# Kernel tuning notes

Measured on AMD Instinct MI355X. Metric: run time of the kernel, lower is better.

## Reference

```python
import jax, jax.numpy as jnp
import numpy as np

BEAM = 4
SOS = 1


def _gru_cell(x, h, Wih, Whh, bih, bhh):
    # x,h: [B,H]; Wih,Whh: [3H,H]; torch GRUCell math
    gi = x @ Wih.T + bih
    gh = h @ Whh.T + bhh
    ir, iz, inn = jnp.split(gi, 3, axis=-1)
    hr, hz, hn = jnp.split(gh, 3, axis=-1)
    r = jax.nn.sigmoid(ir + hr)
    z = jax.nn.sigmoid(iz + hz)
    n = jnp.tanh(inn + r * hn)
    return (1.0 - z) * n + z * h


def setup_inputs() -> dict:
    key = jax.random.key(0)
    V, H, S, L = 32000, 1024, 256, 48
    ks = jax.random.split(key, 10)
    p = lambda k, shape: (jax.random.normal(k, shape, jnp.float32) * 0.02)
    return {
        "input_seq": jax.random.randint(ks[0], (S, 1), 0, V),
        "input_length": S,
        "max_length": L,
        "emb": p(ks[1], (V, H)),
        "enc_Wih": p(ks[2], (3 * H, H)),
        "enc_Whh": p(ks[3], (3 * H, H)),
        "enc_bih": jnp.zeros((3 * H,), jnp.float32),
        "enc_bhh": jnp.zeros((3 * H,), jnp.float32),
        "dec_Wih": p(ks[4], (3 * H, H)),
        "dec_Whh": p(ks[5], (3 * H, H)),
        "dec_bih": jnp.zeros((3 * H,), jnp.float32),
        "dec_bhh": jnp.zeros((3 * H,), jnp.float32),
        "Wc": p(ks[6], (H, 2 * H)),
        "Wout": p(ks[7], (V, H)),
    }


def _beam_search(input_seq, max_length, emb, enc_Wih, enc_Whh, enc_bih, enc_bhh,
                 dec_Wih, dec_Whh, dec_bih, dec_bhh, Wc, Wout):
    H = emb.shape[1]
    # ---- encoder: single-layer GRU over [S] tokens ----
    seq_emb = emb[input_seq[:, 0]]  # [S,H]

    def enc_step(h, x):
        hn = _gru_cell(x[None, :], h, enc_Wih, enc_Whh, enc_bih, enc_bhh)
        return hn, hn[0]

    h0 = jnp.zeros((1, H), emb.dtype)
    h_final, enc_out = jax.lax.scan(enc_step, h0, seq_emb)  # enc_out: [S,H]

    # ---- beam state (all beams start from encoder final hidden, SOS token) ----
    h = jnp.tile(h_final, (BEAM, 1))            # [4,H]
    inputs = jnp.full((BEAM,), SOS, jnp.int32)  # [4]
    cum = jnp.zeros((BEAM,), emb.dtype)
    tokens = jnp.zeros((BEAM, max_length), jnp.int32)
    shist = jnp.zeros((BEAM, max_length), emb.dtype)

    def dec_step(carry, step):
        h, inputs, cum, tokens, shist = carry
        x = emb[inputs]                                     # [4,H]
        hnew = _gru_cell(x, h, dec_Wih, dec_Whh, dec_bih, dec_bhh)  # [4,H]
        # Luong dot attention over encoder outputs
        attn = jax.nn.softmax(jnp.einsum('sh,bh->bs', enc_out, hnew), axis=-1)
        ctx = attn @ enc_out                                # [4,H]
        concat = jnp.tanh(jnp.concatenate([hnew, ctx], axis=-1) @ Wc.T)
        logp = jax.nn.log_softmax(concat @ Wout.T, axis=-1)  # [4,V]
        tp, ti = jax.lax.top_k(logp, BEAM)                  # [4,4]
        # step 0: only beam 0 expands (all beams identical), as in original
        valid = jnp.where(step == 0, jnp.arange(BEAM) == 0,
                          jnp.ones((BEAM,), bool))
        cand = jnp.where(valid[:, None], cum[:, None] + tp, -jnp.inf).reshape(-1)
        sel_scores, sel = jax.lax.top_k(cand, BEAM)         # [4]
        bi = sel // BEAM   # parent beam index i
        jj = sel % BEAM    # topk column index j
        # Faithful to original bug: new hidden indexed by column j, not parent i
        new_h = hnew[jj]
        new_inputs = ti[bi, jj]
        step_scores = tp[bi, jj]
        new_tokens = tokens[bi].at[:, step].set(new_inputs)
        new_shist = shist[bi].at[:, step].set(step_scores)
        return (new_h, new_inputs, sel_scores, new_tokens, new_shist), None

    (h, inputs, cum, tokens, shist), _ = jax.lax.scan(
        dec_step, (h, inputs, cum, tokens, shist), jnp.arange(max_length))
    best = jnp.argmax(cum)  # all beams same length -> avg == cum ranking
    return tokens[best], shist[best]


def reference(input_seq, input_length, max_length, emb, enc_Wih, enc_Whh,
              enc_bih, enc_bhh, dec_Wih, dec_Whh, dec_bih, dec_bhh, Wc, Wout):
    # input_length: full sequence is used (original packs to input_length;
    # here input_length == seq_len)
    return _beam_search(input_seq, max_length, emb, enc_Wih, enc_Whh, enc_bih,
                        enc_bhh, dec_Wih, dec_Whh, dec_bih, dec_bhh, Wc, Wout)
```

## Files before the change

kernel.cpp:

```cpp
#include <hip/hip_runtime.h>
#include <hip/hip_bf16.h>

#define HDIM 1024
#define G3   3072
#define CHK  16
#define NEG_INF (-__builtin_inff())

typedef unsigned short u16;
typedef unsigned int   u32;

__device__ __forceinline__ float bf2f(u32 h){ union{u32 u; float f;} t; t.u = h<<16; return t.f; }

__device__ __forceinline__ float wred_sum(float v){
  #pragma unroll
  for(int o=32;o;o>>=1) v += __shfl_xor(v,o,64);
  return v;
}
__device__ __forceinline__ float wred_max(float v){
  #pragma unroll
  for(int o=32;o;o>>=1) v = fmaxf(v,__shfl_xor(v,o,64));
  return v;
}

__device__ __forceinline__ void load16w(const void* W, long long eoff, int bf, float* x){
  if(bf){
    const uint4* q = (const uint4*)((const u16*)W + eoff);
    uint4 a = q[0], b = q[1];
    x[0]=bf2f(a.x&0xffffu); x[1]=bf2f(a.x>>16);
    x[2]=bf2f(a.y&0xffffu); x[3]=bf2f(a.y>>16);
    x[4]=bf2f(a.z&0xffffu); x[5]=bf2f(a.z>>16);
    x[6]=bf2f(a.w&0xffffu); x[7]=bf2f(a.w>>16);
    x[8]=bf2f(b.x&0xffffu); x[9]=bf2f(b.x>>16);
    x[10]=bf2f(b.y&0xffffu); x[11]=bf2f(b.y>>16);
    x[12]=bf2f(b.z&0xffffu); x[13]=bf2f(b.z>>16);
    x[14]=bf2f(b.w&0xffffu); x[15]=bf2f(b.w>>16);
  } else {
    const float4* q = (const float4*)((const float*)W + eoff);
    float4 A=q[0],B=q[1],C=q[2],D=q[3];
    x[0]=A.x;x[1]=A.y;x[2]=A.z;x[3]=A.w;
    x[4]=B.x;x[5]=B.y;x[6]=B.z;x[7]=B.w;
    x[8]=C.x;x[9]=C.y;x[10]=C.z;x[11]=C.w;
    x[12]=D.x;x[13]=D.y;x[14]=D.z;x[15]=D.w;
  }
}
__device__ __forceinline__ void load16f(const float* p, float* x){
  const float4* q=(const float4*)p;
  float4 A=q[0],B=q[1],C=q[2],D=q[3];
  x[0]=A.x;x[1]=A.y;x[2]=A.z;x[3]=A.w;
  x[4]=B.x;x[5]=B.y;x[6]=B.z;x[7]=B.w;
  x[8]=C.x;x[9]=C.y;x[10]=C.z;x[11]=C.w;
  x[12]=D.x;x[13]=D.y;x[14]=D.z;x[15]=D.w;
}
__device__ __forceinline__ float loadscal(const void* p, long long i, int bf){
  return bf ? bf2f(((const u16*)p)[i]) : ((const float*)p)[i];
}
__device__ __forceinline__ float sigf(float x){ return 1.f/(1.f+expf(-x)); }

__device__ __forceinline__ void dot4_accum(const float* w, const float xr[4][16], float a[4]){
  #pragma unroll
  for(int i=0;i<16;i++){
    a[0] += w[i]*xr[0][i];
    a[1] += w[i]*xr[1][i];
    a[2] += w[i]*xr[2][i];
    a[3] += w[i]*xr[3][i];
  }
}

__device__ __forceinline__ void insert4(float* v, int* ix, float nv, int ni){
  bool b3 = (nv>v[3]) || (nv==v[3] && ni<ix[3]);
  if(!b3) return;
  bool b2 = (nv>v[2]) || (nv==v[2] && ni<ix[2]);
  bool b1 = (nv>v[1]) || (nv==v[1] && ni<ix[1]);
  bool b0 = (nv>v[0]) || (nv==v[0] && ni<ix[0]);
  if(b0){ v[3]=v[2];ix[3]=ix[2]; v[2]=v[1];ix[2]=ix[1]; v[1]=v[0];ix[1]=ix[0]; v[0]=nv;ix[0]=ni; }
  else if(b1){ v[3]=v[2];ix[3]=ix[2]; v[2]=v[1];ix[2]=ix[1]; v[1]=nv;ix[1]=ni; }
  else if(b2){ v[3]=v[2];ix[3]=ix[2]; v[2]=nv;ix[2]=ni; }
  else { v[3]=nv; ix[3]=ni; }
}
__device__ __forceinline__ void merge4(const float* va, const int* ia, const float* vb, const int* ib, float* vo, int* io){
  int pa=0, pb=0;
  for(int k=0;k<4;k++){
    bool ta;
    if(pa>=4) ta=false;
    else if(pb>=4) ta=true;
    else ta = (va[pa]>vb[pb]) || (va[pa]==vb[pb] && ia[pa]<ib[pb]);
    if(ta){ vo[k]=va[pa]; io[k]=ia[pa]; pa++; }
    else  { vo[k]=vb[pb]; io[k]=ib[pb]; pb++; }
  }
}

__global__ __launch_bounds__(256) void k_probe(const u16* emb, int* flag){
  __shared__ int cnt;
  if(threadIdx.x==0) cnt=0;
  __syncthreads();
  int c=0;
  for(int i=threadIdx.x;i<4096;i+=256){
    u32 e = (emb[i]>>7)&0xffu;
    if(e>=0x85u) c++;
  }
  atomicAdd(&cnt,c);
  __syncthreads();
  if(threadIdx.x==0) *flag = (cnt<100)?1:0;
}

__global__ __launch_bounds__(256) void k_enc_gi(const int* seq, const void* emb, const void* Wih,
                                                const void* bih, const int* flag, float* gi){
  int bf = *flag;
  int wg = blockIdx.x; int tg = wg>>3, rg = wg&7;
  int wave = threadIdx.x>>6, lane = threadIdx.x&63;
  int tok[4];
  #pragma unroll
  for(int j=0;j<4;j++) tok[j] = seq[tg*4+j];
  float xr[4][16];
  #pragma unroll
  for(int j=0;j<4;j++) load16w(emb, (long long)tok[j]*HDIM + lane*CHK, bf, xr[j]);
  for(int k=0;k<96;k++){
    int row = rg*384 + wave*96 + k;
    float w[16]; load16w(Wih, (long long)row*HDIM + lane*CHK, bf, w);
    float a[4]={0.f,0.f,0.f,0.f};
    dot4_accum(w, xr, a);
    float bias = loadscal(bih, row, bf);
    #pragma unroll
    for(int b=0;b<4;b++){
      float v = wred_sum(a[b]);
      if(lane==b) gi[(long long)(tg*4+b)*G3 + row] = v + bias;
    }
  }
}

__global__ __launch_bounds__(256) void k_enc_step(const void* Whh, const void* bhh, const int* flag,
                                                  const float* gi, float* enc_out, int t){
  int bf = *flag;
  __shared__ float gh[96];
  int wave = threadIdx.x>>6, lane = threadIdx.x&63;
  int base = blockIdx.x*32;
  float xr[16];
  if(t>0){
    load16f(enc_out + (long long)(t-1)*HDIM + lane*CHK, xr);
  } else {
    #pragma unroll
    for(int i=0;i<16;i++) xr[i]=0.f;
  }
  for(int k=0;k<24;k++){
    int idx = wave*24+k;
    int g = idx>>5, d = idx&31;
    int row = g*HDIM + base + d;
    float w[16]; load16w(Whh,(long long)row*HDIM+lane*CHK,bf,w);
    float a=0.f;
    #pragma unroll
    for(int i=0;i<16;i++) a += w[i]*xr[i];
    a = wred_sum(a);
    if(lane==0) gh[idx] = a + loadscal(bhh,row,bf);
  }
  __syncthreads();
  if(threadIdx.x<32){
    int d = threadIdx.x;
    const float* gir = gi + (long long)t*G3;
    float ir = gir[base+d], iz = gir[HDIM+base+d], in_ = gir[2*HDIM+base+d];
    float hr = gh[d], hz = gh[32+d], hn = gh[64+d];
    float r = sigf(ir+hr);
    float z = sigf(iz+hz);
    float n = tanhf(in_ + r*hn);
    float hp = (t>0) ? enc_out[(long long)(t-1)*HDIM + base+d] : 0.f;
    enc_out[(long long)t*HDIM + base+d] = (1.f-z)*n + z*hp;
  }
}

__global__ __launch_bounds__(256) void k_dec_init(const float* enc_out, int S, float* h_cur, float* cum,
                                                  int* cur_in, int* tokens, float* shist, int L){
  int t = threadIdx.x;
  const float* hf = enc_out + (long long)(S-1)*HDIM;
  for(int i=t;i<4*HDIM;i+=256) h_cur[i] = hf[i&(HDIM-1)];
  if(t<4){ cum[t]=0.f; cur_in[t]=1; }
  for(int i=t;i<4*L;i+=256){ tokens[i]=0; shist[i]=0.f; }
}

__global__ __launch_bounds__(256) void k_dec_gru(const void* emb, const void* Wih, const void* Whh,
                                                 const void* bih, const void* bhh, const int* flag,
                                                 const int* cur_in, const float* h_cur, float* hnew){
  int bf = *flag;
  __shared__ float gibuf[96], ghbuf[96];
  int wave = threadIdx.x>>6, lane = threadIdx.x&63;
  int base = blockIdx.x*8;
  float xr[4][16];
  int tok[4];
  #pragma unroll
  for(int b=0;b<4;b++) tok[b]=cur_in[b];
  #pragma unroll
  for(int b=0;b<4;b++) load16w(emb,(long long)tok[b]*HDIM+lane*CHK,bf,xr[b]);
  for(int k=0;k<6;k++){
    int idx = wave*6+k; int g = idx>>3, d = idx&7;
    int row = g*HDIM + base + d;
    float w[16]; load16w(Wih,(long long)row*HDIM+lane*CHK,bf,w);
    float a[4]={0.f,0.f,0.f,0.f};
    dot4_accum(w,xr,a);
    float bias = loadscal(bih,row,bf);
    #pragma unroll
    for(int b=0;b<4;b++){
      float v = wred_sum(a[b]);
      if(lane==b) gibuf[idx*4+b] = v + bias;
    }
  }
  #pragma unroll
  for(int b=0;b<4;b++) load16f(h_cur+(long long)b*HDIM+lane*CHK, xr[b]);
  for(int k=0;k<6;k++){
    int idx = wave*6+k; int g = idx>>3, d = idx&7;
    int row = g*HDIM + base + d;
    float w[16]; load16w(Whh,(long long)row*HDIM+lane*CHK,bf,w);
    float a[4]={0.f,0.f,0.f,0.f};
    dot4_accum(w,xr,a);
    float bias = loadscal(bhh,row,bf);
    #pragma unroll
    for(int b=0;b<4;b++){
      float v = wred_sum(a[b]);
      if(lane==b) ghbuf[idx*4+b] = v + bias;
    }
  }
  __syncthreads();
  if(threadIdx.x<32){
    int d = threadIdx.x&7, b = threadIdx.x>>3;
    float ir = gibuf[(0*8+d)*4+b], iz = gibuf[(1*8+d)*4+b], in_ = gibuf[(2*8+d)*4+b];
    float hr = ghbuf[(0*8+d)*4+b], hz = ghbuf[(1*8+d)*4+b], hn = ghbuf[(2*8+d)*4+b];
    float r = sigf(ir+hr);
    float z = sigf(iz+hz);
    float n = tanhf(in_ + r*hn);
    float h = h_cur[b*HDIM + base + d];
    hnew[b*HDIM + base + d] = (1.f-z)*n + z*h;
  }
}

__global__ __launch_bounds__(256) void k_dec_scores(const float* enc_out, const float* hnew, float* scores){
  int wave = threadIdx.x>>6, lane = threadIdx.x&63;
  float xr[4][16];
  #pragma unroll
  for(int b=0;b<4;b++) load16f(hnew+(long long)b*HDIM+lane*CHK, xr[b]);
  for(int k=0;k<4;k++){
    int s = (blockIdx.x*4+wave)*4+k;
    float w[16]; load16f(enc_out+(long long)s*HDIM+lane*CHK, w);
    float a[4]={0.f,0.f,0.f,0.f};
    dot4_accum(w,xr,a);
    #pragma unroll
    for(int b=0;b<4;b++){
      float v = wred_sum(a[b]);
      if(lane==b) scores[s*4+b] = v;
    }
  }
}

__global__ __launch_bounds__(256) void k_dec_attnctx(const float* enc_out, const float* scores_g,
                                                     float* ctx, int S){
  __shared__ float sc[256*4];
  int t = threadIdx.x;
  for(int i=t;i<S*4;i+=256) sc[i]=scores_g[i];
  __syncthreads();
  int wave = t>>6, lane = t&63;
  {
    int b = wave;
    float v[4];
    #pragma unroll
    for(int k=0;k<4;k++) v[k]=sc[(lane+64*k)*4+b];
    float m = fmaxf(fmaxf(v[0],v[1]),fmaxf(v[2],v[3]));
    m = wred_max(m);
    float e[4]; float ss=0.f;
    #pragma unroll
    for(int k=0;k<4;k++){ e[k]=expf(v[k]-m); ss+=e[k]; }
    ss = wred_sum(ss);
    #pragma unroll
    for(int k=0;k<4;k++) sc[(lane+64*k)*4+b] = e[k]/ss;
  }
  __syncthreads();
  int hl = t&127, bp = t>>7;
  int h = blockIdx.x*128 + hl;
  int b0 = bp*2;
  float a0=0.f, a1=0.f;
  for(int s=0;s<S;s++){
    float e = enc_out[(long long)s*HDIM + h];
    a0 += sc[s*4+b0]*e;
    a1 += sc[s*4+b0+1]*e;
  }
  ctx[b0*HDIM+h]=a0; ctx[(b0+1)*HDIM+h]=a1;
}

__global__ __launch_bounds__(256) void k_dec_wc(const void* Wc, const int* flag, const float* hnew,
                                                const float* ctx, float* concat){
  int bf = *flag;
  int wave = threadIdx.x>>6, lane = threadIdx.x&63;
  int r0 = blockIdx.x*16 + wave*4;
  float xr[4][16];
  #pragma unroll
  for(int b=0;b<4;b++) load16f(hnew+(long long)b*HDIM+lane*CHK, xr[b]);
  float acc[4][4];
  #pragma unroll
  for(int k=0;k<4;k++){
    #pragma unroll
    for(int b=0;b<4;b++) acc[k][b]=0.f;
  }
  #pragma unroll
  for(int k=0;k<4;k++){
    float w[16]; load16w(Wc,(long long)(r0+k)*2048 + lane*CHK, bf, w);
    #pragma unroll
    for(int i=0;i<16;i++){
      acc[k][0]+=w[i]*xr[0][i]; acc[k][1]+=w[i]*xr[1][i];
      acc[k][2]+=w[i]*xr[2][i]; acc[k][3]+=w[i]*xr[3][i];
    }
  }
  #pragma unroll
  for(int b=0;b<4;b++) load16f(ctx+(long long)b*HDIM+lane*CHK, xr[b]);
  #pragma unroll
  for(int k=0;k<4;k++){
    float w[16]; load16w(Wc,(long long)(r0+k)*2048 + 1024 + lane*CHK, bf, w);
    #pragma unroll
    for(int i=0;i<16;i++){
      acc[k][0]+=w[i]*xr[0][i]; acc[k][1]+=w[i]*xr[1][i];
      acc[k][2]+=w[i]*xr[2][i]; acc[k][3]+=w[i]*xr[3][i];
    }
  }
  #pragma unroll
  for(int k=0;k<4;k++){
    #pragma unroll
    for(int b=0;b<4;b++){
      float v = wred_sum(acc[k][b]);
      if(lane == k*4+b) concat[b*HDIM + r0 + k] = tanhf(v);
    }
  }
}

__global__ __launch_bounds__(256) void k_dec_logits(const void* Wout, const int* flag, const float* concat,
                                                    float* pm, float* ps, float* ptv, int* pti, int V){
  int bf = *flag;
  int wave = threadIdx.x>>6, lane = threadIdx.x&63;
  float xr[4][16];
  #pragma unroll
  for(int b=0;b<4;b++) load16f(concat+(long long)b*HDIM+lane*CHK, xr[b]);
  int wbase = blockIdx.x*125;
  int off = wave*31 + (wave>0?1:0);
  int cnt = (wave==0)?32:31;
  float m[4], s[4], tv[4][4]; int ti_[4][4];
  #pragma unroll
  for(int b=0;b<4;b++){
    m[b]=NEG_INF; s[b]=0.f;
    #pragma unroll
    for(int j=0;j<4;j++){ tv[b][j]=NEG_INF; ti_[b][j]=0; }
  }
  for(int k=0;k<cnt;k++){
    int row = wbase + off + k;
    if(row>=V) break;
    float w[16]; load16w(Wout,(long long)row*HDIM+lane*CHK,bf,w);
    float a[4]={0.f,0.f,0.f,0.f};
    dot4_accum(w,xr,a);
    a[0]=wred_sum(a[0]); a[1]=wred_sum(a[1]); a[2]=wred_sum(a[2]); a[3]=wred_sum(a[3]);
    if(lane==0){
      #pragma unroll
      for(int b=0;b<4;b++){
        float v = a[b];
        if(v>m[b]){ s[b]=s[b]*expf(m[b]-v)+1.f; m[b]=v; }
        else s[b] += expf(v-m[b]);
        insert4(tv[b], ti_[b], v, row);
      }
    }
  }
  __shared__ float lm[16], lssum[16], ltv[64]; __shared__ int lti[64];
  if(lane==0){
    #pragma unroll
    for(int b=0;b<4;b++){
      lm[wave*4+b]=m[b]; lssum[wave*4+b]=s[b];
      #pragma unroll
      for(int j=0;j<4;j++){ ltv[(wave*4+b)*4+j]=tv[b][j]; lti[(wave*4+b)*4+j]=ti_[b][j]; }
    }
  }
  __syncthreads();
  if(threadIdx.x==0){
    for(int b=0;b<4;b++){
      float M=NEG_INF;
      for(int w=0;w<4;w++) M=fmaxf(M,lm[w*4+b]);
      float S=0.f;
      for(int w=0;w<4;w++) S += lssum[w*4+b]*expf(lm[w*4+b]-M);
      float cv[4]; int ci[4];
      for(int j=0;j<4;j++){ cv[j]=ltv[(0*4+b)*4+j]; ci[j]=lti[(0*4+b)*4+j]; }
      for(int w=1;w<4;w++){
        float vo[4]; int io[4];
        merge4(cv,ci,&ltv[(w*4+b)*4],&lti[(w*4+b)*4],vo,io);
        for(int j=0;j<4;j++){ cv[j]=vo[j]; ci[j]=io[j]; }
      }
      pm[blockIdx.x*4+b]=M; ps[blockIdx.x*4+b]=S;
      for(int j=0;j<4;j++){ ptv[(blockIdx.x*4+b)*4+j]=cv[j]; pti[(blockIdx.x*4+b)*4+j]=ci[j]; }
    }
  }
}

__global__ __launch_bounds__(256) void k_dec_finalize(const float* pm, const float* ps, const float* ptv,
                                                      const int* pti, const float* hnew, float* h_cur,
                                                      float* cum, int* cur_in, int* tokens, float* shist,
                                                      int step, int L, const int* flag, void* dout){
  __shared__ float red[256];
  __shared__ float tpv[4][4]; __shared__ int tpi[4][4];
  __shared__ float logZ[4];
  __shared__ float mtv[256*4]; __shared__ int mti[256*4];
  __shared__ int l_bi[4], l_jj[4], l_tok[4]; __shared__ float l_ss[4], l_cum[4];
  __shared__ int otok[4*64]; __shared__ float oshi[4*64];
  __shared__ int bbest;
  int t = threadIdx.x;

  for(int b=0;b<4;b++){
    float v = pm[t*4+b];
    red[t]=v; __syncthreads();
    for(int st=128;st;st>>=1){ if(t<st) red[t]=fmaxf(red[t],red[t+st]); __syncthreads(); }
    float M = red[0]; __syncthreads();
    red[t] = ps[t*4+b]*expf(v-M); __syncthreads();
    for(int st=128;st;st>>=1){ if(t<st) red[t]+=red[t+st]; __syncthreads(); }
    if(t==0) logZ[b]=M+logf(red[0]);
    __syncthreads();
  }
  for(int b=0;b<4;b++){
    for(int j=0;j<4;j++){ mtv[t*4+j]=ptv[(t*4+b)*4+j]; mti[t*4+j]=pti[(t*4+b)*4+j]; }
    __syncthreads();
    for(int st=1; st<256; st<<=1){
      if((t & (2*st-1))==0 && t+st<256){
        float vo[4]; int io[4];
        merge4(&mtv[t*4], &mti[t*4], &mtv[(t+st)*4], &mti[(t+st)*4], vo, io);
        for(int j=0;j<4;j++){ mtv[t*4+j]=vo[j]; mti[t*4+j]=io[j]; }
      }
      __syncthreads();
    }
    if(t<4){ tpv[b][t]=mtv[t]-logZ[b]; tpi[b][t]=mti[t]; }
    __syncthreads();
  }
  if(t==0){
    float oc[4];
    for(int b=0;b<4;b++) oc[b]=cum[b];
    float cand[16];
    for(int b=0;b<4;b++)
      for(int j=0;j<4;j++){
        bool valid = (step>0)||(b==0);
        cand[b*4+j] = valid ? oc[b]+tpv[b][j] : NEG_INF;
      }
    bool used[16];
    for(int i=0;i<16;i++) used[i]=false;
    for(int q=0;q<4;q++){
      int best=0; float bv=NEG_INF;
      for(int i=0;i<16;i++){ if(!used[i] && cand[i]>bv){ bv=cand[i]; best=i; } }
      used[best]=true;
      int bi = best>>2, jj = best&3;
      l_bi[q]=bi; l_jj[q]=jj; l_tok[q]=tpi[bi][jj]; l_ss[q]=tpv[bi][jj]; l_cum[q]=bv;
    }
  }
  __syncthreads();
  for(int i=t;i<4*L;i+=256){ otok[i]=tokens[i]; oshi[i]=shist[i]; }
  __syncthreads();
  for(int i=t;i<4*L;i+=256){
    int q=i/L, c=i%L;
    int src=l_bi[q];
    tokens[i] = (c==step)? l_tok[q] : otok[src*L+c];
    shist[i]  = (c==step)? l_ss[q]  : oshi[src*L+c];
  }
  if(t<4){ cum[t]=l_cum[t]; cur_in[t]=l_tok[t]; }
  for(int i=t;i<4*HDIM;i+=256){
    int q=i>>10;
    h_cur[i] = hnew[l_jj[q]*HDIM + (i&(HDIM-1))];
  }
  if(step==L-1){
    if(t==0){
      int bb=0; float bv=l_cum[0];
      for(int b=1;b<4;b++) if(l_cum[b]>bv){ bv=l_cum[b]; bb=b; }
      bbest=bb;
    }
    __syncthreads();
    int bb=bbest; int bf=*flag;
    for(int c=t;c<L;c+=256){
      float tokv = (float)((c==step)? l_tok[bb] : otok[l_bi[bb]*L+c]);
      float shv  = (c==step)? l_ss[bb] : oshi[l_bi[bb]*L+c];
      if(bf){
        __hip_bfloat16* o = (__hip_bfloat16*)dout;
        o[c]   = __float2bfloat16(tokv);
        o[L+c] = __float2bfloat16(shv);
      } else {
        float* o = (float*)dout;
        o[c]   = tokv;
        o[L+c] = shv;
      }
    }
  }
}

extern "C" void kernel_launch(void* const* d_in, const int* in_sizes, int n_in,
                              void* d_out, int out_size, void* d_ws, size_t ws_size,
                              hipStream_t stream) {
  const int* seq   = (const int*)d_in[0];
  const void* emb  = d_in[3];
  const void* eWih = d_in[4]; const void* eWhh = d_in[5];
  const void* ebih = d_in[6]; const void* ebhh = d_in[7];
  const void* dWih = d_in[8]; const void* dWhh = d_in[9];
  const void* dbih = d_in[10]; const void* dbhh = d_in[11];
  const void* Wc   = d_in[12]; const void* Wout = d_in[13];

  int S = in_sizes[0];
  int L = out_size/2;
  int V = in_sizes[13]/HDIM;

  char* p = (char*)d_ws;
  auto carve = [&](size_t bytes)->void* {
    void* r = (void*)p;
    p += (bytes + 255) & ~(size_t)255;
    return r;
  };
  int*   flag    = (int*)  carve(4);
  float* gi_enc  = (float*)carve((size_t)S*G3*4);
  float* enc_out = (float*)carve((size_t)S*HDIM*4);
  float* h_cur   = (float*)carve(4*HDIM*4);
  float* hnew    = (float*)carve(4*HDIM*4);
  float* scoresb = (float*)carve((size_t)S*4*4);
  float* ctx     = (float*)carve(4*HDIM*4);
  float* concat  = (float*)carve(4*HDIM*4);
  float* pm      = (float*)carve(256*4*4);
  float* ps      = (float*)carve(256*4*4);
  float* ptv     = (float*)carve(256*16*4);
  int*   pti     = (int*)  carve(256*16*4);
  float* cum     = (float*)carve(4*4);
  int*   cur_in  = (int*)  carve(4*4);
  int*   tokens  = (int*)  carve(4*L*4);
  float* shist   = (float*)carve(4*L*4);

  k_probe<<<1,256,0,stream>>>((const u16*)emb, flag);
  k_enc_gi<<<(S/4)*8,256,0,stream>>>(seq, emb, eWih, ebih, flag, gi_enc);
  for(int t=0;t<S;t++)
    k_enc_step<<<32,256,0,stream>>>(eWhh, ebhh, flag, gi_enc, enc_out, t);
  k_dec_init<<<1,256,0,stream>>>(enc_out, S, h_cur, cum, cur_in, tokens, shist, L);
  for(int st=0;st<L;st++){
    k_dec_gru<<<128,256,0,stream>>>(emb, dWih, dWhh, dbih, dbhh, flag, cur_in, h_cur, hnew);
    k_dec_scores<<<16,256,0,stream>>>(enc_out, hnew, scoresb);
    k_dec_attnctx<<<8,256,0,stream>>>(enc_out, scoresb, ctx, S);
    k_dec_wc<<<64,256,0,stream>>>(Wc, flag, hnew, ctx, concat);
    k_dec_logits<<<256,256,0,stream>>>(Wout, flag, concat, pm, ps, ptv, pti, V);
    k_dec_finalize<<<1,256,0,stream>>>(pm, ps, ptv, pti, hnew, h_cur, cum, cur_in,
                                       tokens, shist, st, L, flag, d_out);
  }
}
```

Before: 11.59 ms.

## Replace per-step encoder launches with persistent grid-barrier kernel; widen logits blocks

The 256 per-timestep encoder GRU launches become one persistent kernel of 32 blocks of 512 threads. Each block keeps its 96 rows of Whh in registers and the blocks synchronise between timesteps with an atomic-counter grid barrier. This is meant to remove launch overhead and the repeated reload of Whh from memory at every step. It relies on all 32 blocks being resident at once, and the register-held weights raise register pressure. Separately, the logits kernel moves from 4 to 8 waves per block to spread its rows across more waves.

```diff
diff --git a/kernel.cpp b/kernel.cpp
--- a/kernel.cpp
+++ b/kernel.cpp
@@ -5,6 +5,7 @@
 #define G3   3072
 #define CHK  16
 #define NEG_INF (-__builtin_inff())
+#define EB   32
 
 typedef unsigned short u16;
 typedef unsigned int   u32;
@@ -89,9 +90,21 @@
   }
 }
 
-__global__ __launch_bounds__(256) void k_probe(const u16* emb, int* flag){
+__device__ __forceinline__ void gbar(int* cnt, int nblk, int it){
+  __syncthreads();
+  if(threadIdx.x==0){
+    __hip_atomic_fetch_add(cnt, 1, __ATOMIC_ACQ_REL, __HIP_MEMORY_SCOPE_AGENT);
+    int target = nblk*it;
+    while(__hip_atomic_load(cnt, __ATOMIC_ACQUIRE, __HIP_MEMORY_SCOPE_AGENT) < target)
+      __builtin_amdgcn_s_sleep(1);
+  }
+  __syncthreads();
+  __builtin_amdgcn_fence(__ATOMIC_ACQUIRE, "agent");
+}
+
+__global__ __launch_bounds__(256) void k_probe(const u16* emb, int* flag, int* bar_cnt){
   __shared__ int cnt;
-  if(threadIdx.x==0) cnt=0;
+  if(threadIdx.x==0){ cnt=0; *bar_cnt=0; }
   __syncthreads();
   int c=0;
   for(int i=threadIdx.x;i<4096;i+=256){
@@ -128,41 +141,58 @@
   }
 }
 
-__global__ __launch_bounds__(256) void k_enc_step(const void* Whh, const void* bhh, const int* flag,
-                                                  const float* gi, float* enc_out, int t){
+__global__ __launch_bounds__(512,2) void k_enc_persist(const void* Whh, const void* bhh,
+                                                       const int* flag, const float* gi,
+                                                       float* enc_out, int S, int* bar_cnt){
   int bf = *flag;
-  __shared__ float gh[96];
   int wave = threadIdx.x>>6, lane = threadIdx.x&63;
-  int base = blockIdx.x*32;
-  float xr[16];
-  if(t>0){
-    load16f(enc_out + (long long)(t-1)*HDIM + lane*CHK, xr);
-  } else {
-    #pragma unroll
-    for(int i=0;i<16;i++) xr[i]=0.f;
-  }
-  for(int k=0;k<24;k++){
-    int idx = wave*24+k;
-    int g = idx>>5, d = idx&31;
-    int row = g*HDIM + base + d;
-    float w[16]; load16w(Whh,(long long)row*HDIM+lane*CHK,bf,w);
-    float a=0.f;
-    #pragma unroll
-    for(int i=0;i<16;i++) a += w[i]*xr[i];
-    a = wred_sum(a);
-    if(lane==0) gh[idx] = a + loadscal(bhh,row,bf);
-  }
-  __syncthreads();
-  if(threadIdx.x<32){
-    int d = threadIdx.x;
-    const float* gir = gi + (long long)t*G3;
-    float ir = gir[base+d], iz = gir[HDIM+base+d], in_ = gir[2*HDIM+base+d];
-    float hr = gh[d], hz = gh[32+d], hn = gh[64+d];
-    float r = sigf(ir+hr);
-    float z = sigf(iz+hz);
-    float n = tanhf(in_ + r*hn);
-    float hp = (t>0) ? enc_out[(long long)(t-1)*HDIM + base+d] : 0.f;
-    enc_out[(long long)t*HDIM + base+d] = (1.f-z)*n + z*hp;
+  int dbase = blockIdx.x*32;
+  __shared__ float gh_s[96];
+  __shared__ float bhh_s[96];
+  if(threadIdx.x<96){
+    int rl = threadIdx.x;
+    int row = (rl>>5)*HDIM + dbase + (rl&31);
+    bhh_s[rl] = loadscal(bhh, row, bf);
+  }
+  float wreg[12][16];
+  #pragma unroll
+  for(int k=0;k<12;k++){
+    int rl = wave*12 + k;
+    int row = (rl>>5)*HDIM + dbase + (rl&31);
+    load16w(Whh, (long long)row*HDIM + lane*CHK, bf, wreg[k]);
+  }
+  __syncthreads();
+
+  for(int t=0;t<S;t++){
+    if(t>0) gbar(bar_cnt, EB, t);
+    float h[16];
+    if(t>0){
+      load16f(enc_out + (long long)(t-1)*HDIM + lane*CHK, h);
+    } else {
+      #pragma unroll
+      for(int i=0;i<16;i++) h[i]=0.f;
+    }
+    #pragma unroll
+    for(int k=0;k<12;k++){
+      float a=0.f;
+      #pragma unroll
+      for(int i=0;i<16;i++) a += wreg[k][i]*h[i];
+      a = wred_sum(a);
+      if(lane==k) gh_s[wave*12+k] = a + bhh_s[wave*12+k];
+    }
+    __syncthreads();
+    if(threadIdx.x<32){
+      int d = threadIdx.x;
+      int gd = dbase + d;
+      const float* gir = gi + (long long)t*G3;
+      float ir = gir[gd], iz = gir[HDIM+gd], in_ = gir[2*HDIM+gd];
+      float hr = gh_s[d], hz = gh_s[32+d], hn = gh_s[64+d];
+      float r = sigf(ir+hr);
+      float z = sigf(iz+hz);
+      float n = tanhf(in_ + r*hn);
+      float hp = (t>0) ? enc_out[(long long)(t-1)*HDIM + gd] : 0.f;
+      enc_out[(long long)t*HDIM + gd] = (1.f-z)*n + z*hp;
+    }
   }
 }
 
@@ -325,7 +355,7 @@
   }
 }
 
-__global__ __launch_bounds__(256) void k_dec_logits(const void* Wout, const int* flag, const float* concat,
+__global__ __launch_bounds__(512) void k_dec_logits(const void* Wout, const int* flag, const float* concat,
                                                     float* pm, float* ps, float* ptv, int* pti, int V){
   int bf = *flag;
   int wave = threadIdx.x>>6, lane = threadIdx.x&63;
@@ -333,8 +363,8 @@
   #pragma unroll
   for(int b=0;b<4;b++) load16f(concat+(long long)b*HDIM+lane*CHK, xr[b]);
   int wbase = blockIdx.x*125;
-  int off = wave*31 + (wave>0?1:0);
-  int cnt = (wave==0)?32:31;
+  int off  = (wave<5) ? wave*16 : 80 + (wave-5)*15;
+  int cnt  = (wave<5) ? 16 : 15;
   float m[4], s[4], tv[4][4]; int ti_[4][4];
   #pragma unroll
   for(int b=0;b<4;b++){
@@ -359,7 +389,7 @@
       }
     }
   }
-  __shared__ float lm[16], lssum[16], ltv[64]; __shared__ int lti[64];
+  __shared__ float lm[32], lssum[32], ltv[128]; __shared__ int lti[128];
   if(lane==0){
     #pragma unroll
     for(int b=0;b<4;b++){
@@ -372,12 +402,12 @@
   if(threadIdx.x==0){
     for(int b=0;b<4;b++){
       float M=NEG_INF;
-      for(int w=0;w<4;w++) M=fmaxf(M,lm[w*4+b]);
+      for(int w=0;w<8;w++) M=fmaxf(M,lm[w*4+b]);
       float S=0.f;
-      for(int w=0;w<4;w++) S += lssum[w*4+b]*expf(lm[w*4+b]-M);
+      for(int w=0;w<8;w++) S += lssum[w*4+b]*expf(lm[w*4+b]-M);
       float cv[4]; int ci[4];
       for(int j=0;j<4;j++){ cv[j]=ltv[(0*4+b)*4+j]; ci[j]=lti[(0*4+b)*4+j]; }
-      for(int w=1;w<4;w++){
+      for(int w=1;w<8;w++){
         float vo[4]; int io[4];
         merge4(cv,ci,&ltv[(w*4+b)*4],&lti[(w*4+b)*4],vo,io);
         for(int j=0;j<4;j++){ cv[j]=vo[j]; ci[j]=io[j]; }
@@ -504,6 +534,7 @@
     return r;
   };
   int*   flag    = (int*)  carve(4);
+  int*   bar_cnt = (int*)  carve(4);
   float* gi_enc  = (float*)carve((size_t)S*G3*4);
   float* enc_out = (float*)carve((size_t)S*HDIM*4);
   float* h_cur   = (float*)carve(4*HDIM*4);
@@ -520,17 +551,16 @@
   int*   tokens  = (int*)  carve(4*L*4);
   float* shist   = (float*)carve(4*L*4);
 
-  k_probe<<<1,256,0,stream>>>((const u16*)emb, flag);
+  k_probe<<<1,256,0,stream>>>((const u16*)emb, flag, bar_cnt);
   k_enc_gi<<<(S/4)*8,256,0,stream>>>(seq, emb, eWih, ebih, flag, gi_enc);
-  for(int t=0;t<S;t++)
-    k_enc_step<<<32,256,0,stream>>>(eWhh, ebhh, flag, gi_enc, enc_out, t);
+  k_enc_persist<<<EB,512,0,stream>>>(eWhh, ebhh, flag, gi_enc, enc_out, S, bar_cnt);
   k_dec_init<<<1,256,0,stream>>>(enc_out, S, h_cur, cum, cur_in, tokens, shist, L);
   for(int st=0;st<L;st++){
     k_dec_gru<<<128,256,0,stream>>>(emb, dWih, dWhh, dbih, dbhh, flag, cur_in, h_cur, hnew);
     k_dec_scores<<<16,256,0,stream>>>(enc_out, hnew, scoresb);
     k_dec_attnctx<<<8,256,0,stream>>>(enc_out, scoresb, ctx, S);
     k_dec_wc<<<64,256,0,stream>>>(Wc, flag, hnew, ctx, concat);
-    k_dec_logits<<<256,256,0,stream>>>(Wout, flag, concat, pm, ps, ptv, pti, V);
+    k_dec_logits<<<256,512,0,stream>>>(Wout, flag, concat, pm, ps, ptv, pti, V);
     k_dec_finalize<<<1,256,0,stream>>>(pm, ps, ptv, pti, hnew, h_cur, cum, cur_in,
                                        tokens, shist, st, L, flag, d_out);
   }
```

After: 9.962 ms. -14.1%, faster.
